# Kernel optimization log

Hardware: AMD Instinct MI355X
Metric: run time of the kernel (lower is better)

Reference implementation:

```python
import jax, jax.numpy as jnp
import numpy as np

NHEAD = 8
HB, WB = 16, 16  # block_size


def _mha(q, k, v, w_in, b_in, w_out, b_out, nhead):
    # q,k,v: [L, B, C] seq-first, like torch.nn.MultiheadAttention (eval mode, no dropout)
    Lq, B, C = q.shape
    d = C // nhead
    wq, wk, wv = jnp.split(w_in, 3, axis=0)
    bq, bk, bv = jnp.split(b_in, 3)
    qh = (q @ wq.T + bq).reshape(Lq, B, nhead, d).transpose(1, 2, 0, 3)        # [B,H,Lq,d]
    kh = (k @ wk.T + bk).reshape(k.shape[0], B, nhead, d).transpose(1, 2, 0, 3)
    vh = (v @ wv.T + bv).reshape(v.shape[0], B, nhead, d).transpose(1, 2, 0, 3)
    scale = 1.0 / jnp.sqrt(jnp.asarray(d, dtype=qh.dtype))
    scores = jnp.einsum('bhqd,bhkd->bhqk', qh * scale, kh)
    attn = jax.nn.softmax(scores, axis=-1)
    out = jnp.einsum('bhqk,bhkd->bhqd', attn, vh)                               # [B,H,Lq,d]
    out = out.transpose(2, 0, 1, 3).reshape(Lq, B, C)
    return out @ w_out.T + b_out


def setup_inputs() -> dict:
    key = jax.random.key(0)
    ks = jax.random.split(key, 12)
    n, c, t, h, w = 2, 256, 2, 64, 64
    q = jax.random.normal(ks[0], (n, c, t, h, w), dtype=jnp.float32)
    k = jax.random.normal(ks[1], (n, c, t, h, w), dtype=jnp.float32)
    v = jax.random.normal(ks[2], (n, c, t, h, w), dtype=jnp.float32)
    pos = jax.random.normal(ks[3], (n, c, t, h, w), dtype=jnp.float32)
    s = 0.02
    wl_in = jax.random.normal(ks[4], (3 * c, c), dtype=jnp.float32) * s
    bl_in = jnp.zeros((3 * c,), dtype=jnp.float32)
    wl_out = jax.random.normal(ks[5], (c, c), dtype=jnp.float32) * s
    bl_out = jnp.zeros((c,), dtype=jnp.float32)
    ws_in = jax.random.normal(ks[6], (3 * c, c), dtype=jnp.float32) * s
    bs_in = jnp.zeros((3 * c,), dtype=jnp.float32)
    ws_out = jax.random.normal(ks[7], (c, c), dtype=jnp.float32) * s
    bs_out = jnp.zeros((c,), dtype=jnp.float32)
    return {"q": q, "k": k, "v": v, "pos": pos,
            "wl_in": wl_in, "bl_in": bl_in, "wl_out": wl_out, "bl_out": bl_out,
            "ws_in": ws_in, "bs_in": bs_in, "ws_out": ws_out, "bs_out": bs_out}


def reference(q, k, v, pos, wl_in, bl_in, wl_out, bl_out, ws_in, bs_in, ws_out, bs_out):
    n, c, t_q, h, w = q.shape
    t_k = k.shape[2]
    bn_h, bn_w = h // HB, w // WB

    def to_long(x, t):
        # [n,c,t,h,w] -> [t*bn_h*bn_w, n*HB*WB, c]
        x = x.reshape(n, c, t, bn_h, HB, bn_w, WB).transpose(2, 3, 5, 0, 4, 6, 1)
        return x.reshape(t * bn_h * bn_w, n * HB * WB, c)

    ql = to_long(q, t_q)
    kl = to_long(k, t_k)
    vl = to_long(v, t_k)
    pl = to_long(pos, t_q)

    v1 = _mha(ql + pl, kl + pl, vl, wl_in, bl_in, wl_out, bl_out, NHEAD)

    def long_to_short(x):
        # [t*bn_h*bn_w, n*HB*WB, c] -> [t*HB*WB, n*bn_h*bn_w, c]
        x = x.reshape(t_q, bn_h, bn_w, n, HB, WB, c).transpose(0, 4, 5, 3, 1, 2, 6)
        return x.reshape(t_q * HB * WB, n * bn_h * bn_w, c)

    v2 = long_to_short(v1)
    ps = long_to_short(pl)

    out = _mha(v2 + ps, v2 + ps, v2, ws_in, bs_in, ws_out, bs_out, NHEAD)
    out = out.reshape(t_q, HB, WB, n, bn_h, bn_w, c).transpose(3, 6, 0, 4, 1, 5, 2)
    return out.reshape(n, c, t_q, h, w)
```

## Files before the change

### kernel.cpp

```cpp
#include <hip/hip_runtime.h>
#include <math.h>


#define SCALE_D32 0.17677669529663687f
#define EXP2_SCALE 0.25508680987930193f
#define GLOBAL_AS __attribute__((address_space(1)))
#define LDS_AS __attribute__((address_space(3)))

typedef short short8 __attribute__((ext_vector_type(8)));
typedef short short4v __attribute__((ext_vector_type(4)));
typedef short short2v __attribute__((ext_vector_type(2)));
typedef float floatx4 __attribute__((ext_vector_type(4)));

__device__ __forceinline__ short f2bf(float f) {
  union { float f; unsigned u; } x;
  x.f = f;
  unsigned r = x.u + 0x7fffu + ((x.u >> 16) & 1u);
  return (short)(r >> 16);
}
__device__ __forceinline__ float bf2f(short s) {
  union { unsigned u; float f; } x;
  x.u = ((unsigned)(unsigned short)s) << 16;
  return x.f;
}

__device__ __forceinline__ int o1s_phys(int q, int ch) {
  return q * 256 + (ch & ~63) + ((((ch >> 3) & 7) ^ (q & 7)) << 3) + (ch & 7);
}

__device__ __forceinline__ void stage_w(short* Wsl, const short* Wg, int kb,
                                        int wave, int lane, int rsub, int csub) {
#pragma unroll
  for (int j = 0; j < 8; ++j) {
    int r0 = (wave * 8 + j) * 8;
    int row = r0 + rsub;
    int c = csub ^ (row & 7);
    const short* gp = Wg + (long)row * 256 + kb * 64 + c * 8;
    short* lp = &Wsl[r0 * 64 + lane * 8];
    __builtin_amdgcn_global_load_lds((const GLOBAL_AS void*)gp,
                                     (LDS_AS void*)lp, 16, 0, 0);
  }
}

__device__ __forceinline__ void stage_tile(short* dst, const short* Xg,
                                           int b1, int tid) {
#pragma unroll
  for (int p = 0; p < 4; ++p) {
    int idx = p * 256 + tid;
    int row = idx >> 5;
    int ch = idx & 31;
    int chs = (ch & ~7) | ((ch & 7) ^ (row & 7));
    const short* gp = Xg + ((long)(row * 512 + b1)) * 256 + chs * 8;
    short* lp = dst + idx * 8;
    __builtin_amdgcn_global_load_lds((const GLOBAL_AS void*)gp,
                                     (LDS_AS void*)lp, 16, 0, 0);
  }
}

__global__ __launch_bounds__(256) void pack_kernel(
    const float* __restrict__ q, const float* __restrict__ k,
    const float* __restrict__ v, const float* __restrict__ pos,
    short* __restrict__ Xp, short* __restrict__ Xq,
    short* __restrict__ Xk, short* __restrict__ Xv,
    const float* __restrict__ wl_in, const float* __restrict__ wl_out,
    const float* __restrict__ ws_in, const float* __restrict__ ws_out,
    short* __restrict__ wbf) {
  __shared__ float tP[64][65];
  __shared__ float tX[64][65];
  int b = blockIdx.x;
  int cb = b & 3;
  int h  = (b >> 2) & 63;
  int nt = b >> 8;
  int n = nt >> 1, t = nt & 1;
  int c0 = cb * 64;
  int bh = h >> 4, ii = h & 15;
  long inbase = (long)n * 2097152 + (long)t * 4096 + (long)h * 64;
  int tx = threadIdx.x & 63;
  int ty = threadIdx.x >> 6;

  for (int cc = ty; cc < 64; cc += 4) {
    long a = inbase + (long)(c0 + cc) * 8192 + tx;
    tP[cc][tx] = pos[a];
    tX[cc][tx] = q[a];
  }
  __syncthreads();
  for (int ww = ty; ww < 64; ww += 4) {
    int bw = ww >> 4, j = ww & 15;
    int m1 = (((t * 4 + bh) * 4 + bw) * 512) + n * 256 + ii * 16 + j;
    long o = (long)m1 * 256 + c0 + tx;
    float pv = tP[tx][ww];
    Xp[o] = f2bf(pv);
    Xq[o] = f2bf(tX[tx][ww] + pv);
  }
  __syncthreads();
  for (int cc = ty; cc < 64; cc += 4) {
    long a = inbase + (long)(c0 + cc) * 8192 + tx;
    tX[cc][tx] = k[a];
  }
  __syncthreads();
  for (int ww = ty; ww < 64; ww += 4) {
    int bw = ww >> 4, j = ww & 15;
    int m1 = (((t * 4 + bh) * 4 + bw) * 512) + n * 256 + ii * 16 + j;
    long o = (long)m1 * 256 + c0 + tx;
    Xk[o] = f2bf(tX[tx][ww] + tP[tx][ww]);
  }
  __syncthreads();
  for (int cc = ty; cc < 64; cc += 4) {
    long a = inbase + (long)(c0 + cc) * 8192 + tx;
    tX[cc][tx] = v[a];
  }
  __syncthreads();
  for (int ww = ty; ww < 64; ww += 4) {
    int bw = ww >> 4, j = ww & 15;
    int m1 = (((t * 4 + bh) * 4 + bw) * 512) + n * 256 + ii * 16 + j;
    long o = (long)m1 * 256 + c0 + tx;
    Xv[o] = f2bf(tX[tx][ww]);
  }
  int idx = (blockIdx.x * 256 + threadIdx.x) * 2;
  const float* wp;
  if (idx < 196608) wp = wl_in + idx;
  else if (idx < 262144) wp = wl_out + (idx - 196608);
  else if (idx < 458752) wp = ws_in + (idx - 262144);
  else wp = ws_out + (idx - 458752);
  float2 wv = *(const float2*)wp;
  wbf[idx] = f2bf(wv.x);
  wbf[idx + 1] = f2bf(wv.y);
}

template <bool OUT32>
__global__ __launch_bounds__(256) void gemm_tri(
    const short* __restrict__ A0, const short* __restrict__ A1,
    const short* __restrict__ A2, const short* __restrict__ W0,
    const float* __restrict__ bias0, void* __restrict__ C0,
    void* __restrict__ C1, void* __restrict__ C2) {
  __shared__ short As[128 * 64];
  __shared__ short Ws[64 * 64];
  int z = blockIdx.z;
  const short* A = (z == 0) ? A0 : ((z == 1) ? A1 : A2);
  const short* Wb = W0 + z * 65536;
  const float* bias = bias0 + z * 256;
  void* Csel = (z == 0) ? C0 : ((z == 1) ? C1 : C2);
  int m0 = blockIdx.x * 128;
  int n0 = blockIdx.y * 64;
  int tid = threadIdx.x;
  int lane = tid & 63, wave = tid >> 6;
  int wm = wave >> 1, wn = wave & 1;
  int l15 = lane & 15, quad = lane >> 4;
  int x7 = l15 & 7;
  int rsub = lane >> 3;
  int csub = lane & 7;

  floatx4 acc[4][2];
#pragma unroll
  for (int mt = 0; mt < 4; ++mt)
#pragma unroll
    for (int nt = 0; nt < 2; ++nt) acc[mt][nt] = (floatx4)(0.f);

  for (int kb = 0; kb < 4; ++kb) {
    int k0 = kb * 64;
    if (kb) __syncthreads();
#pragma unroll
    for (int j = 0; j < 4; ++j) {
      int r0 = (wave * 4 + j) * 8;
      int row = r0 + rsub;
      int c = csub ^ (row & 7);
      const short* gp = A + (long)(m0 + row) * 256 + k0 + c * 8;
      short* lp = &As[r0 * 64 + lane * 8];
      __builtin_amdgcn_global_load_lds((const GLOBAL_AS void*)gp,
                                       (LDS_AS void*)lp, 16, 0, 0);
    }
#pragma unroll
    for (int j = 0; j < 2; ++j) {
      int r0 = (wave * 2 + j) * 8;
      int row = r0 + rsub;
      int c = csub ^ (row & 7);
      const short* gp = Wb + (long)(n0 + row) * 256 + k0 + c * 8;
      short* lp = &Ws[r0 * 64 + lane * 8];
      __builtin_amdgcn_global_load_lds((const GLOBAL_AS void*)gp,
                                       (LDS_AS void*)lp, 16, 0, 0);
    }
    __syncthreads();
#pragma unroll
    for (int ks = 0; ks < 2; ++ks) {
      int pc = (ks * 4 + quad) ^ x7;
      short8 af[4], bfr[2];
#pragma unroll
      for (int mt = 0; mt < 4; ++mt) {
        int row = wm * 64 + mt * 16 + l15;
        af[mt] = *(const short8*)&As[row * 64 + pc * 8];
      }
#pragma unroll
      for (int nt = 0; nt < 2; ++nt) {
        int row = wn * 32 + nt * 16 + l15;
        bfr[nt] = *(const short8*)&Ws[row * 64 + pc * 8];
      }
#pragma unroll
      for (int mt = 0; mt < 4; ++mt)
#pragma unroll
        for (int nt = 0; nt < 2; ++nt)
          acc[mt][nt] = __builtin_amdgcn_mfma_f32_16x16x32_bf16(
              af[mt], bfr[nt], acc[mt][nt], 0, 0, 0);
    }
  }
  float bia0 = bias[n0 + wn * 32 + l15];
  float bia1 = bias[n0 + wn * 32 + 16 + l15];
#pragma unroll
  for (int mt = 0; mt < 4; ++mt) {
#pragma unroll
    for (int r = 0; r < 4; ++r) {
      int row = m0 + wm * 64 + mt * 16 + quad * 4 + r;
      long base = (long)row * 256 + n0 + wn * 32 + l15;
      if (OUT32) {
        float* C = (float*)Csel;
        C[base] = acc[mt][0][r] + bia0;
        C[base + 16] = acc[mt][1][r] + bia1;
      } else {
        short* C = (short*)Csel;
        C[base] = f2bf(acc[mt][0][r] + bia0);
        C[base + 16] = f2bf(acc[mt][1][r] + bia1);
      }
    }
  }
}

__global__ __launch_bounds__(256) void attn1_giga(
    const short* __restrict__ Xq, const short* __restrict__ Xk,
    const short* __restrict__ Xv, const short* __restrict__ Xp,
    const short* __restrict__ Wlin, const float* __restrict__ bias_lin,
    const short* __restrict__ Wo, const float* __restrict__ bias_o,
    const short* __restrict__ Wsin, const float* __restrict__ bias_sin,
    short* __restrict__ Q2, short* __restrict__ K2, short* __restrict__ V2) {
  __shared__ short R1[32 * 256];
  __shared__ short R2[32 * 256];
  __shared__ short R3[32 * 256];
  __shared__ short R4[256 * 64];
  int b1 = blockIdx.x;
  int tid = threadIdx.x;
  int wave = tid >> 6, lane = tid & 63;
  int l15 = lane & 15, quad = lane >> 4;
  int x7 = l15 & 7;
  int rsub = lane >> 3;
  int csub = lane & 7;

  floatx4 acc[2][4];

#pragma unroll 1
  for (int z = 0; z < 3; ++z) {
    short* Rz = (z == 0) ? R1 : ((z == 1) ? R2 : R3);
    const short* Xg = (z == 0) ? Xq : ((z == 1) ? Xk : Xv);
    const short* Wz = Wlin + z * 65536;
    stage_tile(Rz, Xg, b1, tid);
#pragma unroll
    for (int mt = 0; mt < 2; ++mt)
#pragma unroll
      for (int nt = 0; nt < 4; ++nt) acc[mt][nt] = (floatx4)(0.f);
    for (int kb = 0; kb < 4; ++kb) {
      __syncthreads();
      stage_w(R4, Wz, kb, wave, lane, rsub, csub);
      __syncthreads();
#pragma unroll
      for (int ks = 0; ks < 2; ++ks) {
        int pc = (ks * 4 + quad) ^ x7;
        short8 af[2], bfr[4];
#pragma unroll
        for (int mt = 0; mt < 2; ++mt)
          af[mt] = *(const short8*)&Rz[(mt * 16 + l15) * 256 + kb * 64 + pc * 8];
#pragma unroll
        for (int nt = 0; nt < 4; ++nt)
          bfr[nt] = *(const short8*)&R4[(wave * 64 + nt * 16 + l15) * 64 + pc * 8];
#pragma unroll
        for (int mt = 0; mt < 2; ++mt)
#pragma unroll
          for (int nt = 0; nt < 4; ++nt)
            acc[mt][nt] = __builtin_amdgcn_mfma_f32_16x16x32_bf16(
                af[mt], bfr[nt], acc[mt][nt], 0, 0, 0);
      }
    }
    __syncthreads();
    float bz[4];
#pragma unroll
    for (int nt = 0; nt < 4; ++nt)
      bz[nt] = bias_lin[z * 256 + wave * 64 + nt * 16 + l15];
#pragma unroll
    for (int mt = 0; mt < 2; ++mt)
#pragma unroll
      for (int r = 0; r < 4; ++r) {
        int row = mt * 16 + quad * 4 + r;
#pragma unroll
        for (int nt = 0; nt < 4; ++nt) {
          int col = wave * 64 + nt * 16 + l15;
          Rz[o1s_phys(row, col)] = f2bf(acc[mt][nt][r] + bz[nt]);
        }
      }
  }
  __syncthreads();

  short* Vtb = R4;
  short* Pwb = R4 + 5120;
  int key = lane & 31;
  int dh = (lane >> 5) * 16;
  int pc2 = 2 * (key & 15) + (key >> 4);

  floatx4 oacc[2][4];
  float lsum[2][2][4];

#pragma unroll
  for (int h2 = 0; h2 < 2; ++h2) {
    int hh = wave * 2 + h2;
    int cb0 = hh * 32 + quad * 8;
    short8 qf0 = *(const short8*)&R1[o1s_phys(l15, cb0)];
    short8 qf1 = *(const short8*)&R1[o1s_phys(l15 + 16, cb0)];
    short8 kf0 = *(const short8*)&R2[o1s_phys(l15, cb0)];
    short8 kf1 = *(const short8*)&R2[o1s_phys(l15 + 16, cb0)];
    short8 v0 = *(const short8*)&R3[o1s_phys(key, hh * 32 + dh)];
    short8 v1 = *(const short8*)&R3[o1s_phys(key, hh * 32 + dh + 8)];
#pragma unroll
    for (int j = 0; j < 8; ++j) {
      Vtb[(wave * 32 + dh + j) * 40 + pc2] = v0[j];
      Vtb[(wave * 32 + dh + 8 + j) * 40 + pc2] = v1[j];
    }
    floatx4 s00 = __builtin_amdgcn_mfma_f32_16x16x32_bf16(qf0, kf0, (floatx4)(0.f), 0, 0, 0);
    floatx4 s01 = __builtin_amdgcn_mfma_f32_16x16x32_bf16(qf0, kf1, (floatx4)(0.f), 0, 0, 0);
    floatx4 s10 = __builtin_amdgcn_mfma_f32_16x16x32_bf16(qf1, kf0, (floatx4)(0.f), 0, 0, 0);
    floatx4 s11 = __builtin_amdgcn_mfma_f32_16x16x32_bf16(qf1, kf1, (floatx4)(0.f), 0, 0, 0);
    float li0[4], li1[4];
#pragma unroll
    for (int r = 0; r < 4; ++r) {
      float p00 = __builtin_amdgcn_exp2f(s00[r] * EXP2_SCALE);
      float p01 = __builtin_amdgcn_exp2f(s01[r] * EXP2_SCALE);
      float p10 = __builtin_amdgcn_exp2f(s10[r] * EXP2_SCALE);
      float p11 = __builtin_amdgcn_exp2f(s11[r] * EXP2_SCALE);
      li0[r] = p00 + p01;
      li1[r] = p10 + p11;
      short2v pa, pb;
      pa.x = f2bf(p00); pa.y = f2bf(p01);
      pb.x = f2bf(p10); pb.y = f2bf(p11);
      *(short2v*)&Pwb[(wave * 32 + quad * 4 + r) * 40 + 2 * l15] = pa;
      *(short2v*)&Pwb[(wave * 32 + 16 + quad * 4 + r) * 40 + 2 * l15] = pb;
    }
#pragma unroll
    for (int r = 0; r < 4; ++r) {
      li0[r] += __shfl_xor(li0[r], 1, 64);
      li0[r] += __shfl_xor(li0[r], 2, 64);
      li0[r] += __shfl_xor(li0[r], 4, 64);
      li0[r] += __shfl_xor(li0[r], 8, 64);
      li1[r] += __shfl_xor(li1[r], 1, 64);
      li1[r] += __shfl_xor(li1[r], 2, 64);
      li1[r] += __shfl_xor(li1[r], 4, 64);
      li1[r] += __shfl_xor(li1[r], 8, 64);
      lsum[h2][0][r] = li0[r];
      lsum[h2][1][r] = li1[r];
    }
    short8 pf0 = *(const short8*)&Pwb[(wave * 32 + l15) * 40 + quad * 8];
    short8 pf1 = *(const short8*)&Pwb[(wave * 32 + 16 + l15) * 40 + quad * 8];
    short8 vt0 = *(const short8*)&Vtb[(wave * 32 + l15) * 40 + quad * 8];
    short8 vt1 = *(const short8*)&Vtb[(wave * 32 + 16 + l15) * 40 + quad * 8];
    oacc[h2][0] = __builtin_amdgcn_mfma_f32_16x16x32_bf16(pf0, vt0, (floatx4)(0.f), 0, 0, 0);
    oacc[h2][1] = __builtin_amdgcn_mfma_f32_16x16x32_bf16(pf0, vt1, (floatx4)(0.f), 0, 0, 0);
    oacc[h2][2] = __builtin_amdgcn_mfma_f32_16x16x32_bf16(pf1, vt0, (floatx4)(0.f), 0, 0, 0);
    oacc[h2][3] = __builtin_amdgcn_mfma_f32_16x16x32_bf16(pf1, vt1, (floatx4)(0.f), 0, 0, 0);
  }

  __syncthreads();

#pragma unroll
  for (int h2 = 0; h2 < 2; ++h2) {
    int hh = wave * 2 + h2;
    int cA = hh * 32 + l15;
    int cB = cA + 16;
#pragma unroll
    for (int r = 0; r < 4; ++r) {
      float inv0 = 1.f / lsum[h2][0][r];
      float inv1 = 1.f / lsum[h2][1][r];
      int qa = quad * 4 + r, qb = 16 + quad * 4 + r;
      R1[o1s_phys(qa, cA)] = f2bf(oacc[h2][0][r] * inv0);
      R1[o1s_phys(qa, cB)] = f2bf(oacc[h2][1][r] * inv0);
      R1[o1s_phys(qb, cA)] = f2bf(oacc[h2][2][r] * inv1);
      R1[o1s_phys(qb, cB)] = f2bf(oacc[h2][3][r] * inv1);
    }
  }

#pragma unroll
  for (int mt = 0; mt < 2; ++mt)
#pragma unroll
    for (int nt = 0; nt < 4; ++nt) acc[mt][nt] = (floatx4)(0.f);
  for (int kb = 0; kb < 4; ++kb) {
    __syncthreads();
    stage_w(R4, Wo, kb, wave, lane, rsub, csub);
    __syncthreads();
#pragma unroll
    for (int ks = 0; ks < 2; ++ks) {
      int pc = (ks * 4 + quad) ^ x7;
      short8 af[2], bfr[4];
#pragma unroll
      for (int mt = 0; mt < 2; ++mt)
        af[mt] = *(const short8*)&R1[(mt * 16 + l15) * 256 + kb * 64 + pc * 8];
#pragma unroll
      for (int nt = 0; nt < 4; ++nt)
        bfr[nt] = *(const short8*)&R4[(wave * 64 + nt * 16 + l15) * 64 + pc * 8];
#pragma unroll
      for (int mt = 0; mt < 2; ++mt)
#pragma unroll
        for (int nt = 0; nt < 4; ++nt)
          acc[mt][nt] = __builtin_amdgcn_mfma_f32_16x16x32_bf16(
              af[mt], bfr[nt], acc[mt][nt], 0, 0, 0);
    }
  }

  __syncthreads();
  {
    float bvo[4];
#pragma unroll
    for (int nt = 0; nt < 4; ++nt) bvo[nt] = bias_o[wave * 64 + nt * 16 + l15];
#pragma unroll
    for (int mt = 0; mt < 2; ++mt) {
#pragma unroll
      for (int r = 0; r < 4; ++r) {
        int qrow = mt * 16 + quad * 4 + r;
        long pbase = ((long)qrow * 512 + b1) * 256;
#pragma unroll
        for (int nt = 0; nt < 4; ++nt) {
          int col = wave * 64 + nt * 16 + l15;
          float val = acc[mt][nt][r] + bvo[nt];
          int ph = o1s_phys(qrow, col);
          R3[ph] = f2bf(val);
          R2[ph] = f2bf(val + bf2f(Xp[pbase + col]));
        }
      }
    }
  }

  int nn = b1 >> 8, ii = (b1 >> 4) & 15, jj = b1 & 15;
#pragma unroll 1
  for (int z = 0; z < 3; ++z) {
    const short* Wz = Wsin + z * 65536;
    const short* Ab = (z < 2) ? R2 : R3;
    short* outz = (z == 0) ? Q2 : ((z == 1) ? K2 : V2);
    float bz[4];
#pragma unroll
    for (int nt = 0; nt < 4; ++nt)
      bz[nt] = bias_sin[z * 256 + wave * 64 + nt * 16 + l15];
#pragma unroll
    for (int mt = 0; mt < 2; ++mt)
#pragma unroll
      for (int nt = 0; nt < 4; ++nt) acc[mt][nt] = (floatx4)(0.f);
    for (int kb = 0; kb < 4; ++kb) {
      __syncthreads();
      stage_w(R4, Wz, kb, wave, lane, rsub, csub);
      __syncthreads();
#pragma unroll
      for (int ks = 0; ks < 2; ++ks) {
        int pc = (ks * 4 + quad) ^ x7;
        short8 af[2], bfr[4];
#pragma unroll
        for (int mt = 0; mt < 2; ++mt)
          af[mt] = *(const short8*)&Ab[(mt * 16 + l15) * 256 + kb * 64 + pc * 8];
#pragma unroll
        for (int nt = 0; nt < 4; ++nt)
          bfr[nt] = *(const short8*)&R4[(wave * 64 + nt * 16 + l15) * 64 + pc * 8];
#pragma unroll
        for (int mt = 0; mt < 2; ++mt)
#pragma unroll
          for (int nt = 0; nt < 4; ++nt)
            acc[mt][nt] = __builtin_amdgcn_mfma_f32_16x16x32_bf16(
                af[mt], bfr[nt], acc[mt][nt], 0, 0, 0);
      }
    }
#pragma unroll
    for (int mt = 0; mt < 2; ++mt) {
#pragma unroll
      for (int r = 0; r < 4; ++r) {
        int qrow = mt * 16 + quad * 4 + r;
        int t = qrow >> 4, bh = (qrow >> 2) & 3, bw = qrow & 3;
        int m2 = (t * 256 + ii * 16 + jj) * 32 + nn * 16 + bh * 4 + bw;
        long xbase = (long)m2 * 256;
#pragma unroll
        for (int nt = 0; nt < 4; ++nt) {
          int col = wave * 64 + nt * 16 + l15;
          outz[xbase + col] = f2bf(acc[mt][nt][r] + bz[nt]);
        }
      }
    }
  }
}

__global__ __launch_bounds__(256) void attn2_mfma(
    const short* __restrict__ Q2, const short* __restrict__ K2,
    const short* __restrict__ V2, short* __restrict__ O2) {
  __shared__ short Ks[64][40];
  __shared__ short Vt[32][72];
  __shared__ short Pw[4][16][72];
  int bid = blockIdx.x;
  int rest = bid & 255;
  int qblk = bid >> 8;
  int hh = 2 * (rest & 3) + (rest >> 7);
  int b2 = (rest >> 2) & 31;
  int tid = threadIdx.x;
  int wave = tid >> 6, lane = tid & 63;
  int l15 = lane & 15, quad = lane >> 4;

  short8 qf;
  {
    long tok = (long)(qblk * 64 + wave * 16 + l15) * 32 + b2;
    qf = *(const short8*)(Q2 + tok * 256 + hh * 32 + quad * 8);
  }
  floatx4 Oa = (floatx4)(0.f), Ob = (floatx4)(0.f);
  float li[4] = {0.f, 0.f, 0.f, 0.f};

  int skey = tid >> 2;
  int sd0 = (tid & 3) * 8;
  int vkey = lane;
  int vd0 = wave * 8;
  int vcol = (vkey & 15) * 4 + (vkey >> 4);

  for (int kb = 0; kb < 8; ++kb) {
    if (kb) __syncthreads();
    {
      long tok = (long)(kb * 64 + skey) * 32 + b2;
      *(short8*)&Ks[skey][sd0] = *(const short8*)(K2 + tok * 256 + hh * 32 + sd0);
    }
    {
      long tok = (long)(kb * 64 + vkey) * 32 + b2;
      short8 v = *(const short8*)(V2 + tok * 256 + hh * 32 + vd0);
#pragma unroll
      for (int j = 0; j < 8; ++j) Vt[vd0 + j][vcol] = v[j];
    }
    __syncthreads();
    floatx4 st[4];
#pragma unroll
    for (int kt = 0; kt < 4; ++kt) {
      short8 kf = *(const short8*)&Ks[kt * 16 + l15][quad * 8];
      st[kt] = __builtin_amdgcn_mfma_f32_16x16x32_bf16(qf, kf, (floatx4)(0.f), 0, 0, 0);
    }
#pragma unroll
    for (int r = 0; r < 4; ++r) {
      float p0 = __builtin_amdgcn_exp2f(st[0][r] * EXP2_SCALE);
      float p1 = __builtin_amdgcn_exp2f(st[1][r] * EXP2_SCALE);
      float p2 = __builtin_amdgcn_exp2f(st[2][r] * EXP2_SCALE);
      float p3 = __builtin_amdgcn_exp2f(st[3][r] * EXP2_SCALE);
      li[r] += (p0 + p1) + (p2 + p3);
      short4v pp;
      pp.x = f2bf(p0); pp.y = f2bf(p1); pp.z = f2bf(p2); pp.w = f2bf(p3);
      *(short4v*)&Pw[wave][quad * 4 + r][l15 * 4] = pp;
    }
#pragma unroll
    for (int kk = 0; kk < 2; ++kk) {
      short8 pf = *(const short8*)&Pw[wave][l15][kk * 32 + quad * 8];
      short8 v0 = *(const short8*)&Vt[l15][kk * 32 + quad * 8];
      short8 v1 = *(const short8*)&Vt[16 + l15][kk * 32 + quad * 8];
      Oa = __builtin_amdgcn_mfma_f32_16x16x32_bf16(pf, v0, Oa, 0, 0, 0);
      Ob = __builtin_amdgcn_mfma_f32_16x16x32_bf16(pf, v1, Ob, 0, 0, 0);
    }
  }
#pragma unroll
  for (int r = 0; r < 4; ++r) {
    float s = li[r];
    s += __shfl_xor(s, 1, 64);
    s += __shfl_xor(s, 2, 64);
    s += __shfl_xor(s, 4, 64);
    s += __shfl_xor(s, 8, 64);
    float inv = 1.f / s;
    long tok = (long)(qblk * 64 + wave * 16 + quad * 4 + r) * 32 + b2;
    long a = tok * 256 + hh * 32 + l15;
    O2[a] = f2bf(Oa[r] * inv);
    O2[a + 16] = f2bf(Ob[r] * inv);
  }
}

__global__ __launch_bounds__(256) void unpack_kernel(
    const float* __restrict__ Y, float* __restrict__ out) {
  __shared__ float tl[64][65];
  int b = blockIdx.x;
  int cb = b & 3;
  int h = (b >> 2) & 63;
  int nt = b >> 8;
  int n = nt >> 1, t = nt & 1;
  int c0 = cb * 64;
  int bh = h >> 4, ii = h & 15;
  int tx = threadIdx.x & 63;
  int ty = threadIdx.x >> 6;
  for (int ww = ty; ww < 64; ww += 4) {
    int bw = ww >> 4, j = ww & 15;
    int l2 = t * 256 + ii * 16 + j;
    int b2 = n * 16 + bh * 4 + bw;
    int m2 = l2 * 32 + b2;
    tl[tx][ww] = Y[(long)m2 * 256 + c0 + tx];
  }
  __syncthreads();
  long ob = (long)n * 2097152 + (long)t * 4096 + (long)h * 64 + tx;
  for (int cc = ty; cc < 64; cc += 4) {
    out[ob + (long)(c0 + cc) * 8192] = tl[cc][tx];
  }
}

extern "C" void kernel_launch(void* const* d_in, const int* in_sizes, int n_in,
                              void* d_out, int out_size, void* d_ws, size_t ws_size,
                              hipStream_t stream) {
  const float* q      = (const float*)d_in[0];
  const float* k      = (const float*)d_in[1];
  const float* v      = (const float*)d_in[2];
  const float* pos    = (const float*)d_in[3];
  const float* wl_in  = (const float*)d_in[4];
  const float* bl_in  = (const float*)d_in[5];
  const float* wl_out = (const float*)d_in[6];
  const float* bl_out = (const float*)d_in[7];
  const float* ws_in  = (const float*)d_in[8];
  const float* bs_in  = (const float*)d_in[9];
  const float* ws_out = (const float*)d_in[10];
  const float* bs_out = (const float*)d_in[11];
  float* out = (float*)d_out;
  char* wsb = (char*)d_ws;
  const size_t SLB = 16777216;
  short* s0 = (short*)(wsb);
  short* wbf = (short*)(wsb + SLB / 2);
  short* s1 = (short*)(wsb + SLB);
  short* s2 = (short*)(wsb + 2 * SLB);
  short* s3 = (short*)(wsb + 3 * SLB);
  short* s4 = (short*)(wsb + 4 * SLB);
  short* s5 = (short*)(wsb + 5 * SLB);
  short* s6 = (short*)(wsb + 6 * SLB);

  pack_kernel<<<1024, 256, 0, stream>>>(q, k, v, pos, s0, s1, s2, s3,
                                        wl_in, wl_out, ws_in, ws_out, wbf);

  attn1_giga<<<512, 256, 0, stream>>>(s1, s2, s3, s0, wbf, bl_in,
                                      wbf + 196608, bl_out,
                                      wbf + 262144, bs_in, s4, s5, s6);

  attn2_mfma<<<2048, 256, 0, stream>>>(s4, s5, s6, s1);
  dim3 g1(128, 4, 1);
  gemm_tri<true><<<g1, 256, 0, stream>>>(s1, s1, s1, wbf + 458752, bs_out,
                                         s2, s2, s2);

  unpack_kernel<<<1024, 256, 0, stream>>>((const float*)s2, out);
}
```

Baseline: 202.8 us.

## Double-buffer weight staging in fused attention kernel GEMMs with cross-GEMM prefetch

Replaces the single-buffer 64-wide weight staging, which synchronised twice per k-block, with a 32-wide double-buffered pipeline. The next weight slice, including the first slice of the following GEMM, is loaded into LDS while MFMAs run on the current one. All three input tiles are also staged up front rather than per projection. This aims to hide global-to-LDS latency and cut barrier count. In exchange, LDS footprint and barrier subtlety go up, since the prefetched next-GEMM slice must survive epilogue writes.

```diff
diff --git a/kernel.cpp b/kernel.cpp
--- a/kernel.cpp
+++ b/kernel.cpp
@@ -39,6 +39,53 @@
     short* lp = &Wsl[r0 * 64 + lane * 8];
     __builtin_amdgcn_global_load_lds((const GLOBAL_AS void*)gp,
                                      (LDS_AS void*)lp, 16, 0, 0);
+  }
+}
+
+__device__ __forceinline__ void stage_w32(short* buf, const short* Wg,
+                                          int kb32, int tid) {
+#pragma unroll
+  for (int j = 0; j < 4; ++j) {
+    int row = j * 64 + (tid >> 2);
+    int c = tid & 3;
+    int cs = c ^ ((row >> 1) & 3);
+    const short* gp = Wg + (long)row * 256 + kb32 * 32 + cs * 8;
+    short* lp = buf + j * 2048 + tid * 8;
+    __builtin_amdgcn_global_load_lds((const GLOBAL_AS void*)gp,
+                                     (LDS_AS void*)lp, 16, 0, 0);
+  }
+}
+
+__device__ __forceinline__ void gemm32_pipe(
+    const short* A, const short* Wg, const short* Wng, bool prestaged,
+    short* bufA, short* bufB, floatx4 (&acc)[2][4],
+    int tid, int wave, int l15, int quad, int x7) {
+  if (!prestaged) {
+    stage_w32(bufA, Wg, 0, tid);
+    __syncthreads();
+  }
+  int pcB = quad ^ ((l15 >> 1) & 3);
+#pragma unroll
+  for (int t = 0; t < 8; ++t) {
+    const short* cur = (t & 1) ? bufB : bufA;
+    short* nxt = (t & 1) ? bufA : bufB;
+    if (t < 7) stage_w32(nxt, Wg, t + 1, tid);
+    else if (Wng) stage_w32(nxt, Wng, 0, tid);
+    int pcA = ((t & 1) * 4 + quad) ^ x7;
+    short8 af[2], bfr[4];
+#pragma unroll
+    for (int mt = 0; mt < 2; ++mt)
+      af[mt] = *(const short8*)&A[(mt * 16 + l15) * 256 + (t >> 1) * 64 + pcA * 8];
+#pragma unroll
+    for (int nt = 0; nt < 4; ++nt)
+      bfr[nt] = *(const short8*)&cur[(wave * 64 + nt * 16 + l15) * 32 + pcB * 8];
+#pragma unroll
+    for (int mt = 0; mt < 2; ++mt)
+#pragma unroll
+      for (int nt = 0; nt < 4; ++nt)
+        acc[mt][nt] = __builtin_amdgcn_mfma_f32_16x16x32_bf16(
+            af[mt], bfr[nt], acc[mt][nt], 0, 0, 0);
+    __syncthreads();
   }
 }
 
@@ -233,50 +280,32 @@
   __shared__ short R1[32 * 256];
   __shared__ short R2[32 * 256];
   __shared__ short R3[32 * 256];
-  __shared__ short R4[256 * 64];
+  __shared__ short R4[2 * 8192];
   int b1 = blockIdx.x;
   int tid = threadIdx.x;
   int wave = tid >> 6, lane = tid & 63;
   int l15 = lane & 15, quad = lane >> 4;
   int x7 = l15 & 7;
-  int rsub = lane >> 3;
-  int csub = lane & 7;
+
+  short* bufA = R4;
+  short* bufB = R4 + 8192;
+
+  stage_tile(R1, Xq, b1, tid);
+  stage_tile(R2, Xk, b1, tid);
+  stage_tile(R3, Xv, b1, tid);
 
   floatx4 acc[2][4];
 
 #pragma unroll 1
   for (int z = 0; z < 3; ++z) {
     short* Rz = (z == 0) ? R1 : ((z == 1) ? R2 : R3);
-    const short* Xg = (z == 0) ? Xq : ((z == 1) ? Xk : Xv);
     const short* Wz = Wlin + z * 65536;
-    stage_tile(Rz, Xg, b1, tid);
+    const short* Wn = (z < 2) ? (Wlin + (z + 1) * 65536) : (const short*)0;
 #pragma unroll
     for (int mt = 0; mt < 2; ++mt)
 #pragma unroll
       for (int nt = 0; nt < 4; ++nt) acc[mt][nt] = (floatx4)(0.f);
-    for (int kb = 0; kb < 4; ++kb) {
-      __syncthreads();
-      stage_w(R4, Wz, kb, wave, lane, rsub, csub);
-      __syncthreads();
-#pragma unroll
-      for (int ks = 0; ks < 2; ++ks) {
-        int pc = (ks * 4 + quad) ^ x7;
-        short8 af[2], bfr[4];
-#pragma unroll
-        for (int mt = 0; mt < 2; ++mt)
-          af[mt] = *(const short8*)&Rz[(mt * 16 + l15) * 256 + kb * 64 + pc * 8];
-#pragma unroll
-        for (int nt = 0; nt < 4; ++nt)
-          bfr[nt] = *(const short8*)&R4[(wave * 64 + nt * 16 + l15) * 64 + pc * 8];
-#pragma unroll
-        for (int mt = 0; mt < 2; ++mt)
-#pragma unroll
-          for (int nt = 0; nt < 4; ++nt)
-            acc[mt][nt] = __builtin_amdgcn_mfma_f32_16x16x32_bf16(
-                af[mt], bfr[nt], acc[mt][nt], 0, 0, 0);
-      }
-    }
-    __syncthreads();
+    gemm32_pipe(Rz, Wz, Wn, z > 0, bufA, bufB, acc, tid, wave, l15, quad, x7);
     float bz[4];
 #pragma unroll
     for (int nt = 0; nt < 4; ++nt)
@@ -363,6 +392,7 @@
 
   __syncthreads();
 
+  stage_w32(bufA, Wo, 0, tid);
 #pragma unroll
   for (int h2 = 0; h2 < 2; ++h2) {
     int hh = wave * 2 + h2;
@@ -379,35 +409,14 @@
       R1[o1s_phys(qb, cB)] = f2bf(oacc[h2][3][r] * inv1);
     }
   }
+  __syncthreads();
 
 #pragma unroll
   for (int mt = 0; mt < 2; ++mt)
 #pragma unroll
     for (int nt = 0; nt < 4; ++nt) acc[mt][nt] = (floatx4)(0.f);
-  for (int kb = 0; kb < 4; ++kb) {
-    __syncthreads();
-    stage_w(R4, Wo, kb, wave, lane, rsub, csub);
-    __syncthreads();
-#pragma unroll
-    for (int ks = 0; ks < 2; ++ks) {
-      int pc = (ks * 4 + quad) ^ x7;
-      short8 af[2], bfr[4];
-#pragma unroll
-      for (int mt = 0; mt < 2; ++mt)
-        af[mt] = *(const short8*)&R1[(mt * 16 + l15) * 256 + kb * 64 + pc * 8];
-#pragma unroll
-      for (int nt = 0; nt < 4; ++nt)
-        bfr[nt] = *(const short8*)&R4[(wave * 64 + nt * 16 + l15) * 64 + pc * 8];
-#pragma unroll
-      for (int mt = 0; mt < 2; ++mt)
-#pragma unroll
-        for (int nt = 0; nt < 4; ++nt)
-          acc[mt][nt] = __builtin_amdgcn_mfma_f32_16x16x32_bf16(
-              af[mt], bfr[nt], acc[mt][nt], 0, 0, 0);
-    }
-  }
-
-  __syncthreads();
+  gemm32_pipe(R1, Wo, Wsin, true, bufA, bufB, acc, tid, wave, l15, quad, x7);
+
   {
     float bvo[4];
 #pragma unroll
@@ -429,11 +438,13 @@
       }
     }
   }
+  __syncthreads();
 
   int nn = b1 >> 8, ii = (b1 >> 4) & 15, jj = b1 & 15;
 #pragma unroll 1
   for (int z = 0; z < 3; ++z) {
     const short* Wz = Wsin + z * 65536;
+    const short* Wn = (z < 2) ? (Wsin + (z + 1) * 65536) : (const short*)0;
     const short* Ab = (z < 2) ? R2 : R3;
     short* outz = (z == 0) ? Q2 : ((z == 1) ? K2 : V2);
     float bz[4];
@@ -444,28 +455,7 @@
     for (int mt = 0; mt < 2; ++mt)
 #pragma unroll
       for (int nt = 0; nt < 4; ++nt) acc[mt][nt] = (floatx4)(0.f);
-    for (int kb = 0; kb < 4; ++kb) {
-      __syncthreads();
-      stage_w(R4, Wz, kb, wave, lane, rsub, csub);
-      __syncthreads();
-#pragma unroll
-      for (int ks = 0; ks < 2; ++ks) {
-        int pc = (ks * 4 + quad) ^ x7;
-        short8 af[2], bfr[4];
-#pragma unroll
-        for (int mt = 0; mt < 2; ++mt)
-          af[mt] = *(const short8*)&Ab[(mt * 16 + l15) * 256 + kb * 64 + pc * 8];
-#pragma unroll
-        for (int nt = 0; nt < 4; ++nt)
-          bfr[nt] = *(const short8*)&R4[(wave * 64 + nt * 16 + l15) * 64 + pc * 8];
-#pragma unroll
-        for (int mt = 0; mt < 2; ++mt)
-#pragma unroll
-          for (int nt = 0; nt < 4; ++nt)
-            acc[mt][nt] = __builtin_amdgcn_mfma_f32_16x16x32_bf16(
-                af[mt], bfr[nt], acc[mt][nt], 0, 0, 0);
-      }
-    }
+    gemm32_pipe(Ab, Wz, Wn, true, bufA, bufB, acc, tid, wave, l15, quad, x7);
 #pragma unroll
     for (int mt = 0; mt < 2; ++mt) {
 #pragma unroll
```

Measured after the change: 207.6 us. 2.4% more time.

## Vectorize pack kernel with full-channel tiles and overlap first Wo stage in attn1

Applied to the files above, without the earlier changes.

The pack kernel now handles all 256 channels per block with 512 threads. It uses float4 global loads and short4 bf16 stores, so the grid drops from 1024 to 256 blocks, each with a much larger LDS tile (about 135 KB). In attn1, the first output-projection weight tile is staged before the normalized attention output is written to LDS, which merges two barriers and overlaps that load with the writes. The main risk is lower occupancy and fewer blocks in flight for the pack stage, plus possible LDS bank conflicts in the strided column reads.

```diff
diff --git a/kernel.cpp b/kernel.cpp
--- a/kernel.cpp
+++ b/kernel.cpp
@@ -57,7 +57,7 @@
   }
 }
 
-__global__ __launch_bounds__(256) void pack_kernel(
+__global__ __launch_bounds__(512) void pack_kernel(
     const float* __restrict__ q, const float* __restrict__ k,
     const float* __restrict__ v, const float* __restrict__ pos,
     short* __restrict__ Xp, short* __restrict__ Xq,
@@ -65,66 +65,95 @@
     const float* __restrict__ wl_in, const float* __restrict__ wl_out,
     const float* __restrict__ ws_in, const float* __restrict__ ws_out,
     short* __restrict__ wbf) {
-  __shared__ float tP[64][65];
-  __shared__ float tX[64][65];
+  __shared__ float tP[256][66];
+  __shared__ float tX[256][66];
   int b = blockIdx.x;
-  int cb = b & 3;
-  int h  = (b >> 2) & 63;
-  int nt = b >> 8;
+  int h = b & 63;
+  int nt = b >> 6;
   int n = nt >> 1, t = nt & 1;
-  int c0 = cb * 64;
   int bh = h >> 4, ii = h & 15;
   long inbase = (long)n * 2097152 + (long)t * 4096 + (long)h * 64;
-  int tx = threadIdx.x & 63;
-  int ty = threadIdx.x >> 6;
-
-  for (int cc = ty; cc < 64; cc += 4) {
-    long a = inbase + (long)(c0 + cc) * 8192 + tx;
-    tP[cc][tx] = pos[a];
-    tX[cc][tx] = q[a];
-  }
-  __syncthreads();
-  for (int ww = ty; ww < 64; ww += 4) {
-    int bw = ww >> 4, j = ww & 15;
-    int m1 = (((t * 4 + bh) * 4 + bw) * 512) + n * 256 + ii * 16 + j;
-    long o = (long)m1 * 256 + c0 + tx;
-    float pv = tP[tx][ww];
-    Xp[o] = f2bf(pv);
-    Xq[o] = f2bf(tX[tx][ww] + pv);
-  }
-  __syncthreads();
-  for (int cc = ty; cc < 64; cc += 4) {
-    long a = inbase + (long)(c0 + cc) * 8192 + tx;
-    tX[cc][tx] = k[a];
-  }
-  __syncthreads();
-  for (int ww = ty; ww < 64; ww += 4) {
-    int bw = ww >> 4, j = ww & 15;
-    int m1 = (((t * 4 + bh) * 4 + bw) * 512) + n * 256 + ii * 16 + j;
-    long o = (long)m1 * 256 + c0 + tx;
-    Xk[o] = f2bf(tX[tx][ww] + tP[tx][ww]);
-  }
-  __syncthreads();
-  for (int cc = ty; cc < 64; cc += 4) {
-    long a = inbase + (long)(c0 + cc) * 8192 + tx;
-    tX[cc][tx] = v[a];
-  }
-  __syncthreads();
-  for (int ww = ty; ww < 64; ww += 4) {
-    int bw = ww >> 4, j = ww & 15;
-    int m1 = (((t * 4 + bh) * 4 + bw) * 512) + n * 256 + ii * 16 + j;
-    long o = (long)m1 * 256 + c0 + tx;
-    Xv[o] = f2bf(tX[tx][ww]);
-  }
-  int idx = (blockIdx.x * 256 + threadIdx.x) * 2;
+  int tid = threadIdx.x;
+  int wv = tid >> 6, lane = tid & 63;
+
+#pragma unroll
+  for (int p = 0; p < 8; ++p) {
+    int idx = p * 512 + tid;
+    int c = idx >> 4;
+    int w4 = (idx & 15) * 4;
+    long a = inbase + (long)c * 8192 + w4;
+    *(float4*)&tP[c][w4] = *(const float4*)&pos[a];
+    *(float4*)&tX[c][w4] = *(const float4*)&q[a];
+  }
+  __syncthreads();
+#pragma unroll
+  for (int p = 0; p < 8; ++p) {
+    int w = p * 8 + wv;
+    int bw = w >> 4, j = w & 15;
+    long m1 = (((t * 4 + bh) * 4 + bw) * 512) + n * 256 + ii * 16 + j;
+    long o = m1 * 256 + lane * 4;
+    short4v xp, xq;
+#pragma unroll
+    for (int s = 0; s < 4; ++s) {
+      float pvv = tP[lane * 4 + s][w];
+      xp[s] = f2bf(pvv);
+      xq[s] = f2bf(tX[lane * 4 + s][w] + pvv);
+    }
+    *(short4v*)&Xp[o] = xp;
+    *(short4v*)&Xq[o] = xq;
+  }
+  __syncthreads();
+#pragma unroll
+  for (int p = 0; p < 8; ++p) {
+    int idx = p * 512 + tid;
+    int c = idx >> 4;
+    int w4 = (idx & 15) * 4;
+    *(float4*)&tX[c][w4] = *(const float4*)&k[inbase + (long)c * 8192 + w4];
+  }
+  __syncthreads();
+#pragma unroll
+  for (int p = 0; p < 8; ++p) {
+    int w = p * 8 + wv;
+    int bw = w >> 4, j = w & 15;
+    long m1 = (((t * 4 + bh) * 4 + bw) * 512) + n * 256 + ii * 16 + j;
+    long o = m1 * 256 + lane * 4;
+    short4v xk;
+#pragma unroll
+    for (int s = 0; s < 4; ++s)
+      xk[s] = f2bf(tX[lane * 4 + s][w] + tP[lane * 4 + s][w]);
+    *(short4v*)&Xk[o] = xk;
+  }
+  __syncthreads();
+#pragma unroll
+  for (int p = 0; p < 8; ++p) {
+    int idx = p * 512 + tid;
+    int c = idx >> 4;
+    int w4 = (idx & 15) * 4;
+    *(float4*)&tX[c][w4] = *(const float4*)&v[inbase + (long)c * 8192 + w4];
+  }
+  __syncthreads();
+#pragma unroll
+  for (int p = 0; p < 8; ++p) {
+    int w = p * 8 + wv;
+    int bw = w >> 4, j = w & 15;
+    long m1 = (((t * 4 + bh) * 4 + bw) * 512) + n * 256 + ii * 16 + j;
+    long o = m1 * 256 + lane * 4;
+    short4v xv;
+#pragma unroll
+    for (int s = 0; s < 4; ++s) xv[s] = f2bf(tX[lane * 4 + s][w]);
+    *(short4v*)&Xv[o] = xv;
+  }
+  int idx = (b * 512 + tid) * 4;
   const float* wp;
   if (idx < 196608) wp = wl_in + idx;
   else if (idx < 262144) wp = wl_out + (idx - 196608);
   else if (idx < 458752) wp = ws_in + (idx - 262144);
   else wp = ws_out + (idx - 458752);
-  float2 wv = *(const float2*)wp;
-  wbf[idx] = f2bf(wv.x);
-  wbf[idx + 1] = f2bf(wv.y);
+  float4 wv4 = *(const float4*)wp;
+  wbf[idx] = f2bf(wv4.x);
+  wbf[idx + 1] = f2bf(wv4.y);
+  wbf[idx + 2] = f2bf(wv4.z);
+  wbf[idx + 3] = f2bf(wv4.w);
 }
 
 template <bool OUT32>
@@ -363,6 +392,7 @@
 
   __syncthreads();
 
+  stage_w(R4, Wo, 0, wave, lane, rsub, csub);
 #pragma unroll
   for (int h2 = 0; h2 < 2; ++h2) {
     int hh = wave * 2 + h2;
@@ -379,15 +409,18 @@
       R1[o1s_phys(qb, cB)] = f2bf(oacc[h2][3][r] * inv1);
     }
   }
+  __syncthreads();
 
 #pragma unroll
   for (int mt = 0; mt < 2; ++mt)
 #pragma unroll
     for (int nt = 0; nt < 4; ++nt) acc[mt][nt] = (floatx4)(0.f);
   for (int kb = 0; kb < 4; ++kb) {
-    __syncthreads();
-    stage_w(R4, Wo, kb, wave, lane, rsub, csub);
-    __syncthreads();
+    if (kb) {
+      __syncthreads();
+      stage_w(R4, Wo, kb, wave, lane, rsub, csub);
+      __syncthreads();
+    }
 #pragma unroll
     for (int ks = 0; ks < 2; ++ks) {
       int pc = (ks * 4 + quad) ^ x7;
@@ -620,8 +653,8 @@
   short* s5 = (short*)(wsb + 5 * SLB);
   short* s6 = (short*)(wsb + 6 * SLB);
 
-  pack_kernel<<<1024, 256, 0, stream>>>(q, k, v, pos, s0, s1, s2, s3,
-                                        wl_in, wl_out, ws_in, ws_out, wbf);
+  pack_kernel<<<256, 512, 0, stream>>>(q, k, v, pos, s0, s1, s2, s3,
+                                       wl_in, wl_out, ws_in, ws_out, wbf);
 
   attn1_giga<<<512, 256, 0, stream>>>(s1, s2, s3, s0, wbf, bl_in,
                                       wbf + 196608, bl_out,
```

New measurement: 205.5 us. No clear change (+1.3%).

## Fuse second attention with output projection into one all-heads kernel

Applied to the files above, without the earlier changes.

Replaces the per-head second attention kernel and the separate output-projection GEMM with one 512-thread kernel. Each block handles all eight heads for 64 queries, stages K/V tiles with async global-to-LDS loads, keeps the attention output in LDS, and applies the output projection with bias in place. This removes a launch and the bf16 round trip of the attention output through global memory. The trade-off is a grid of only 256 blocks with heavy LDS use, so occupancy is lower. Separately, attn1 now prefetches the first Wo tile before its epilogue writes to overlap that load.

```diff
diff --git a/kernel.cpp b/kernel.cpp
--- a/kernel.cpp
+++ b/kernel.cpp
@@ -39,6 +39,20 @@
     short* lp = &Wsl[r0 * 64 + lane * 8];
     __builtin_amdgcn_global_load_lds((const GLOBAL_AS void*)gp,
                                      (LDS_AS void*)lp, 16, 0, 0);
+  }
+}
+
+__device__ __forceinline__ void stage_w512(short* Ws, const short* Wg,
+                                           int kb, int tid) {
+#pragma unroll
+  for (int j = 0; j < 4; ++j) {
+    int idx = j * 512 + tid;
+    int row = idx >> 3;
+    int c = idx & 7;
+    int cs = c ^ (row & 7);
+    const short* gp = Wg + (long)row * 256 + kb * 64 + cs * 8;
+    __builtin_amdgcn_global_load_lds((const GLOBAL_AS void*)gp,
+                                     (LDS_AS void*)(Ws + idx * 8), 16, 0, 0);
   }
 }
 
@@ -127,102 +141,6 @@
   wbf[idx + 1] = f2bf(wv.y);
 }
 
-template <bool OUT32>
-__global__ __launch_bounds__(256) void gemm_tri(
-    const short* __restrict__ A0, const short* __restrict__ A1,
-    const short* __restrict__ A2, const short* __restrict__ W0,
-    const float* __restrict__ bias0, void* __restrict__ C0,
-    void* __restrict__ C1, void* __restrict__ C2) {
-  __shared__ short As[128 * 64];
-  __shared__ short Ws[64 * 64];
-  int z = blockIdx.z;
-  const short* A = (z == 0) ? A0 : ((z == 1) ? A1 : A2);
-  const short* Wb = W0 + z * 65536;
-  const float* bias = bias0 + z * 256;
-  void* Csel = (z == 0) ? C0 : ((z == 1) ? C1 : C2);
-  int m0 = blockIdx.x * 128;
-  int n0 = blockIdx.y * 64;
-  int tid = threadIdx.x;
-  int lane = tid & 63, wave = tid >> 6;
-  int wm = wave >> 1, wn = wave & 1;
-  int l15 = lane & 15, quad = lane >> 4;
-  int x7 = l15 & 7;
-  int rsub = lane >> 3;
-  int csub = lane & 7;
-
-  floatx4 acc[4][2];
-#pragma unroll
-  for (int mt = 0; mt < 4; ++mt)
-#pragma unroll
-    for (int nt = 0; nt < 2; ++nt) acc[mt][nt] = (floatx4)(0.f);
-
-  for (int kb = 0; kb < 4; ++kb) {
-    int k0 = kb * 64;
-    if (kb) __syncthreads();
-#pragma unroll
-    for (int j = 0; j < 4; ++j) {
-      int r0 = (wave * 4 + j) * 8;
-      int row = r0 + rsub;
-      int c = csub ^ (row & 7);
-      const short* gp = A + (long)(m0 + row) * 256 + k0 + c * 8;
-      short* lp = &As[r0 * 64 + lane * 8];
-      __builtin_amdgcn_global_load_lds((const GLOBAL_AS void*)gp,
-                                       (LDS_AS void*)lp, 16, 0, 0);
-    }
-#pragma unroll
-    for (int j = 0; j < 2; ++j) {
-      int r0 = (wave * 2 + j) * 8;
-      int row = r0 + rsub;
-      int c = csub ^ (row & 7);
-      const short* gp = Wb + (long)(n0 + row) * 256 + k0 + c * 8;
-      short* lp = &Ws[r0 * 64 + lane * 8];
-      __builtin_amdgcn_global_load_lds((const GLOBAL_AS void*)gp,
-                                       (LDS_AS void*)lp, 16, 0, 0);
-    }
-    __syncthreads();
-#pragma unroll
-    for (int ks = 0; ks < 2; ++ks) {
-      int pc = (ks * 4 + quad) ^ x7;
-      short8 af[4], bfr[2];
-#pragma unroll
-      for (int mt = 0; mt < 4; ++mt) {
-        int row = wm * 64 + mt * 16 + l15;
-        af[mt] = *(const short8*)&As[row * 64 + pc * 8];
-      }
-#pragma unroll
-      for (int nt = 0; nt < 2; ++nt) {
-        int row = wn * 32 + nt * 16 + l15;
-        bfr[nt] = *(const short8*)&Ws[row * 64 + pc * 8];
-      }
-#pragma unroll
-      for (int mt = 0; mt < 4; ++mt)
-#pragma unroll
-        for (int nt = 0; nt < 2; ++nt)
-          acc[mt][nt] = __builtin_amdgcn_mfma_f32_16x16x32_bf16(
-              af[mt], bfr[nt], acc[mt][nt], 0, 0, 0);
-    }
-  }
-  float bia0 = bias[n0 + wn * 32 + l15];
-  float bia1 = bias[n0 + wn * 32 + 16 + l15];
-#pragma unroll
-  for (int mt = 0; mt < 4; ++mt) {
-#pragma unroll
-    for (int r = 0; r < 4; ++r) {
-      int row = m0 + wm * 64 + mt * 16 + quad * 4 + r;
-      long base = (long)row * 256 + n0 + wn * 32 + l15;
-      if (OUT32) {
-        float* C = (float*)Csel;
-        C[base] = acc[mt][0][r] + bia0;
-        C[base + 16] = acc[mt][1][r] + bia1;
-      } else {
-        short* C = (short*)Csel;
-        C[base] = f2bf(acc[mt][0][r] + bia0);
-        C[base + 16] = f2bf(acc[mt][1][r] + bia1);
-      }
-    }
-  }
-}
-
 __global__ __launch_bounds__(256) void attn1_giga(
     const short* __restrict__ Xq, const short* __restrict__ Xk,
     const short* __restrict__ Xv, const short* __restrict__ Xp,
@@ -363,6 +281,7 @@
 
   __syncthreads();
 
+  stage_w(R4, Wo, 0, wave, lane, rsub, csub);
 #pragma unroll
   for (int h2 = 0; h2 < 2; ++h2) {
     int hh = wave * 2 + h2;
@@ -379,15 +298,18 @@
       R1[o1s_phys(qb, cB)] = f2bf(oacc[h2][3][r] * inv1);
     }
   }
+  __syncthreads();
 
 #pragma unroll
   for (int mt = 0; mt < 2; ++mt)
 #pragma unroll
     for (int nt = 0; nt < 4; ++nt) acc[mt][nt] = (floatx4)(0.f);
   for (int kb = 0; kb < 4; ++kb) {
-    __syncthreads();
-    stage_w(R4, Wo, kb, wave, lane, rsub, csub);
-    __syncthreads();
+    if (kb) {
+      __syncthreads();
+      stage_w(R4, Wo, kb, wave, lane, rsub, csub);
+      __syncthreads();
+    }
 #pragma unroll
     for (int ks = 0; ks < 2; ++ks) {
       int pc = (ks * 4 + quad) ^ x7;
@@ -484,87 +406,169 @@
   }
 }
 
-__global__ __launch_bounds__(256) void attn2_mfma(
+__global__ __launch_bounds__(512) void attn2_mega(
     const short* __restrict__ Q2, const short* __restrict__ K2,
-    const short* __restrict__ V2, short* __restrict__ O2) {
-  __shared__ short Ks[64][40];
-  __shared__ short Vt[32][72];
-  __shared__ short Pw[4][16][72];
+    const short* __restrict__ V2, const short* __restrict__ Wout,
+    const float* __restrict__ bias_out, float* __restrict__ Yf) {
+  __shared__ union {
+    struct {
+      short Ks[32 * 256];
+      short Vs[32 * 256];
+      short Vt[8 * 32 * 40];
+      short Pw[8 * 64 * 40];
+    } a;
+    struct {
+      short O2s[64 * 256];
+      short Ws[256 * 64];
+    } g;
+  } u;
   int bid = blockIdx.x;
-  int rest = bid & 255;
-  int qblk = bid >> 8;
-  int hh = 2 * (rest & 3) + (rest >> 7);
-  int b2 = (rest >> 2) & 31;
+  int qblk = bid >> 5, b2 = bid & 31;
   int tid = threadIdx.x;
-  int wave = tid >> 6, lane = tid & 63;
+  int hh = tid >> 6, lane = tid & 63;
   int l15 = lane & 15, quad = lane >> 4;
-
-  short8 qf;
-  {
-    long tok = (long)(qblk * 64 + wave * 16 + l15) * 32 + b2;
-    qf = *(const short8*)(Q2 + tok * 256 + hh * 32 + quad * 8);
-  }
-  floatx4 Oa = (floatx4)(0.f), Ob = (floatx4)(0.f);
-  float li[4] = {0.f, 0.f, 0.f, 0.f};
-
-  int skey = tid >> 2;
-  int sd0 = (tid & 3) * 8;
-  int vkey = lane;
-  int vd0 = wave * 8;
-  int vcol = (vkey & 15) * 4 + (vkey >> 4);
-
-  for (int kb = 0; kb < 8; ++kb) {
+  int x7 = l15 & 7;
+
+  short8 qf[4];
+#pragma unroll
+  for (int qt = 0; qt < 4; ++qt) {
+    long tok = (long)(qblk * 64 + qt * 16 + l15) * 32 + b2;
+    qf[qt] = *(const short8*)(Q2 + tok * 256 + hh * 32 + quad * 8);
+  }
+
+  floatx4 Oa[4][2];
+#pragma unroll
+  for (int qt = 0; qt < 4; ++qt) {
+    Oa[qt][0] = (floatx4)(0.f);
+    Oa[qt][1] = (floatx4)(0.f);
+  }
+  float li[4][4];
+#pragma unroll
+  for (int qt = 0; qt < 4; ++qt)
+#pragma unroll
+    for (int r = 0; r < 4; ++r) li[qt][r] = 0.f;
+
+  int key = lane & 31;
+  int dh = (lane >> 5) * 16;
+  int pc2 = 2 * (key & 15) + (key >> 4);
+  int lcv0 = hh * 4 + (dh >> 3);
+  int pv0 = (lcv0 & ~7) | ((lcv0 & 7) ^ (key & 7));
+  int lcv1 = lcv0 + 1;
+  int pv1 = (lcv1 & ~7) | ((lcv1 & 7) ^ (key & 7));
+  int lcK = hh * 4 + quad;
+  int pk = (lcK & ~7) | ((lcK & 7) ^ x7);
+
+  for (int kb = 0; kb < 16; ++kb) {
     if (kb) __syncthreads();
+#pragma unroll
+    for (int p = 0; p < 2; ++p) {
+      int idx = p * 512 + tid;
+      int row = idx >> 5, ch = idx & 31;
+      int chs = (ch & ~7) | ((ch & 7) ^ (row & 7));
+      long src = ((long)((kb * 32 + row) * 32 + b2)) * 256 + chs * 8;
+      __builtin_amdgcn_global_load_lds((const GLOBAL_AS void*)(K2 + src),
+                                       (LDS_AS void*)(u.a.Ks + idx * 8), 16, 0, 0);
+      __builtin_amdgcn_global_load_lds((const GLOBAL_AS void*)(V2 + src),
+                                       (LDS_AS void*)(u.a.Vs + idx * 8), 16, 0, 0);
+    }
+    __syncthreads();
     {
-      long tok = (long)(kb * 64 + skey) * 32 + b2;
-      *(short8*)&Ks[skey][sd0] = *(const short8*)(K2 + tok * 256 + hh * 32 + sd0);
-    }
-    {
-      long tok = (long)(kb * 64 + vkey) * 32 + b2;
-      short8 v = *(const short8*)(V2 + tok * 256 + hh * 32 + vd0);
-#pragma unroll
-      for (int j = 0; j < 8; ++j) Vt[vd0 + j][vcol] = v[j];
-    }
+      short8 v0 = *(const short8*)&u.a.Vs[key * 256 + pv0 * 8];
+      short8 v1 = *(const short8*)&u.a.Vs[key * 256 + pv1 * 8];
+#pragma unroll
+      for (int j = 0; j < 8; ++j) {
+        u.a.Vt[(hh * 32 + dh + j) * 40 + pc2] = v0[j];
+        u.a.Vt[(hh * 32 + dh + 8 + j) * 40 + pc2] = v1[j];
+      }
+    }
+    short8 kf0 = *(const short8*)&u.a.Ks[l15 * 256 + pk * 8];
+    short8 kf1 = *(const short8*)&u.a.Ks[(16 + l15) * 256 + pk * 8];
+#pragma unroll
+    for (int qt = 0; qt < 4; ++qt) {
+      floatx4 s0 = __builtin_amdgcn_mfma_f32_16x16x32_bf16(qf[qt], kf0, (floatx4)(0.f), 0, 0, 0);
+      floatx4 s1 = __builtin_amdgcn_mfma_f32_16x16x32_bf16(qf[qt], kf1, (floatx4)(0.f), 0, 0, 0);
+#pragma unroll
+      for (int r = 0; r < 4; ++r) {
+        float p0 = __builtin_amdgcn_exp2f(s0[r] * EXP2_SCALE);
+        float p1 = __builtin_amdgcn_exp2f(s1[r] * EXP2_SCALE);
+        li[qt][r] += p0 + p1;
+        short2v pa;
+        pa.x = f2bf(p0); pa.y = f2bf(p1);
+        *(short2v*)&u.a.Pw[(hh * 64 + qt * 16 + quad * 4 + r) * 40 + 2 * l15] = pa;
+      }
+    }
+    short8 vt0 = *(const short8*)&u.a.Vt[(hh * 32 + l15) * 40 + quad * 8];
+    short8 vt1 = *(const short8*)&u.a.Vt[(hh * 32 + 16 + l15) * 40 + quad * 8];
+#pragma unroll
+    for (int qt = 0; qt < 4; ++qt) {
+      short8 pf = *(const short8*)&u.a.Pw[(hh * 64 + qt * 16 + l15) * 40 + quad * 8];
+      Oa[qt][0] = __builtin_amdgcn_mfma_f32_16x16x32_bf16(pf, vt0, Oa[qt][0], 0, 0, 0);
+      Oa[qt][1] = __builtin_amdgcn_mfma_f32_16x16x32_bf16(pf, vt1, Oa[qt][1], 0, 0, 0);
+    }
+  }
+
+#pragma unroll
+  for (int qt = 0; qt < 4; ++qt)
+#pragma unroll
+    for (int r = 0; r < 4; ++r) {
+      float s = li[qt][r];
+      s += __shfl_xor(s, 1, 64);
+      s += __shfl_xor(s, 2, 64);
+      s += __shfl_xor(s, 4, 64);
+      s += __shfl_xor(s, 8, 64);
+      li[qt][r] = s;
+    }
+
+  __syncthreads();
+
+#pragma unroll
+  for (int qt = 0; qt < 4; ++qt)
+#pragma unroll
+    for (int r = 0; r < 4; ++r) {
+      float inv = 1.f / li[qt][r];
+      int q = qt * 16 + quad * 4 + r;
+      u.g.O2s[o1s_phys(q, hh * 32 + l15)] = f2bf(Oa[qt][0][r] * inv);
+      u.g.O2s[o1s_phys(q, hh * 32 + 16 + l15)] = f2bf(Oa[qt][1][r] * inv);
+    }
+
+  floatx4 acc[4][2];
+#pragma unroll
+  for (int mt = 0; mt < 4; ++mt) {
+    acc[mt][0] = (floatx4)(0.f);
+    acc[mt][1] = (floatx4)(0.f);
+  }
+  for (int kb = 0; kb < 4; ++kb) {
     __syncthreads();
-    floatx4 st[4];
-#pragma unroll
-    for (int kt = 0; kt < 4; ++kt) {
-      short8 kf = *(const short8*)&Ks[kt * 16 + l15][quad * 8];
-      st[kt] = __builtin_amdgcn_mfma_f32_16x16x32_bf16(qf, kf, (floatx4)(0.f), 0, 0, 0);
-    }
+    stage_w512(u.g.Ws, Wout, kb, tid);
+    __syncthreads();
+#pragma unroll
+    for (int ks = 0; ks < 2; ++ks) {
+      int pc = (ks * 4 + quad) ^ x7;
+      short8 af[4], bfr[2];
+#pragma unroll
+      for (int mt = 0; mt < 4; ++mt)
+        af[mt] = *(const short8*)&u.g.O2s[(mt * 16 + l15) * 256 + kb * 64 + pc * 8];
+#pragma unroll
+      for (int nt = 0; nt < 2; ++nt)
+        bfr[nt] = *(const short8*)&u.g.Ws[(hh * 32 + nt * 16 + l15) * 64 + pc * 8];
+#pragma unroll
+      for (int mt = 0; mt < 4; ++mt)
+#pragma unroll
+        for (int nt = 0; nt < 2; ++nt)
+          acc[mt][nt] = __builtin_amdgcn_mfma_f32_16x16x32_bf16(
+              af[mt], bfr[nt], acc[mt][nt], 0, 0, 0);
+    }
+  }
+  float bo0 = bias_out[hh * 32 + l15];
+  float bo1 = bias_out[hh * 32 + 16 + l15];
+#pragma unroll
+  for (int mt = 0; mt < 4; ++mt)
 #pragma unroll
     for (int r = 0; r < 4; ++r) {
-      float p0 = __builtin_amdgcn_exp2f(st[0][r] * EXP2_SCALE);
-      float p1 = __builtin_amdgcn_exp2f(st[1][r] * EXP2_SCALE);
-      float p2 = __builtin_amdgcn_exp2f(st[2][r] * EXP2_SCALE);
-      float p3 = __builtin_amdgcn_exp2f(st[3][r] * EXP2_SCALE);
-      li[r] += (p0 + p1) + (p2 + p3);
-      short4v pp;
-      pp.x = f2bf(p0); pp.y = f2bf(p1); pp.z = f2bf(p2); pp.w = f2bf(p3);
-      *(short4v*)&Pw[wave][quad * 4 + r][l15 * 4] = pp;
-    }
-#pragma unroll
-    for (int kk = 0; kk < 2; ++kk) {
-      short8 pf = *(const short8*)&Pw[wave][l15][kk * 32 + quad * 8];
-      short8 v0 = *(const short8*)&Vt[l15][kk * 32 + quad * 8];
-      short8 v1 = *(const short8*)&Vt[16 + l15][kk * 32 + quad * 8];
-      Oa = __builtin_amdgcn_mfma_f32_16x16x32_bf16(pf, v0, Oa, 0, 0, 0);
-      Ob = __builtin_amdgcn_mfma_f32_16x16x32_bf16(pf, v1, Ob, 0, 0, 0);
-    }
-  }
-#pragma unroll
-  for (int r = 0; r < 4; ++r) {
-    float s = li[r];
-    s += __shfl_xor(s, 1, 64);
-    s += __shfl_xor(s, 2, 64);
-    s += __shfl_xor(s, 4, 64);
-    s += __shfl_xor(s, 8, 64);
-    float inv = 1.f / s;
-    long tok = (long)(qblk * 64 + wave * 16 + quad * 4 + r) * 32 + b2;
-    long a = tok * 256 + hh * 32 + l15;
-    O2[a] = f2bf(Oa[r] * inv);
-    O2[a + 16] = f2bf(Ob[r] * inv);
-  }
+      long tok = (long)(qblk * 64 + mt * 16 + quad * 4 + r) * 32 + b2;
+      Yf[tok * 256 + hh * 32 + l15] = acc[mt][0][r] + bo0;
+      Yf[tok * 256 + hh * 32 + 16 + l15] = acc[mt][1][r] + bo1;
+    }
 }
 
 __global__ __launch_bounds__(256) void unpack_kernel(
@@ -627,10 +631,8 @@
                                       wbf + 196608, bl_out,
                                       wbf + 262144, bs_in, s4, s5, s6);
 
-  attn2_mfma<<<2048, 256, 0, stream>>>(s4, s5, s6, s1);
-  dim3 g1(128, 4, 1);
-  gemm_tri<true><<<g1, 256, 0, stream>>>(s1, s1, s1, wbf + 458752, bs_out,
-                                         s2, s2, s2);
+  attn2_mega<<<256, 512, 0, stream>>>(s4, s5, s6, wbf + 458752, bs_out,
+                                      (float*)s2);
 
   unpack_kernel<<<1024, 256, 0, stream>>>((const float*)s2, out);
 }
```

Measured after the change: 210.1 us. 3.6% more time.
